# Optimization experiments

Measured on AMD Instinct MI355X. Metric: run time of the kernel, lower is better.

The kernel has to match this reference:

```python
import jax, jax.numpy as jnp
import numpy as np

CL = 256   # context_length (global in original code)
IL = 64    # inst_length (global in original code)
PC, CH1, CH2, CH3 = 64, 128, 256, 256
CK1, CK2, CK3 = 3, 3, 3
CS1, CS2, CS3 = 1, 2, 2
CP1, CP2, CP3 = 1, 1, 1
BCH1, BCH2, BCH3 = 64, 128, 256
F1, OUT = 1024, 2
B = 2048
C3_OUT = 64 * CH3            # 16384, per __init__ formula with CL-1=255
F1_IN = C3_OUT + BCH3        # 16640


def _conv1d(x, W, b, stride, pad):
    # x: [B, Cin, L], W: [Cout, Cin, K]
    y = jax.lax.conv_general_dilated(x, W, window_strides=(stride,),
                                     padding=[(pad, pad)],
                                     dimension_numbers=("NCH", "OIH", "NCH"))
    return y + b[None, :, None]


def setup_inputs() -> dict:
    key = jax.random.key(0)
    ks = jax.random.split(key, 20)
    s = lambda *sh: 1.0 / np.sqrt(np.prod(sh[1:]))
    def w(k, *sh):
        return jax.random.normal(k, sh, dtype=jnp.float32) * s(*sh)
    return {
        "x": jax.random.normal(ks[0], (B, CL * IL), dtype=jnp.float32),
        "Wp": w(ks[1], PC, IL, 2), "bp": jnp.zeros((PC,), jnp.float32),
        "W1": w(ks[2], CH1, PC, CK1), "b1": jnp.zeros((CH1,), jnp.float32),
        "W2": w(ks[3], CH2, CH1, CK2), "b2": jnp.zeros((CH2,), jnp.float32),
        "W3": w(ks[4], CH3, CH2, CK3), "b3": jnp.zeros((CH3,), jnp.float32),
        "Wb1": w(ks[5], BCH1, IL), "bb1": jnp.zeros((BCH1,), jnp.float32),
        "Wb2": w(ks[6], BCH2, BCH1), "bb2": jnp.zeros((BCH2,), jnp.float32),
        "Wb3": w(ks[7], BCH3, BCH2), "bb3": jnp.zeros((BCH3,), jnp.float32),
        "Wfc1": w(ks[8], F1, F1_IN), "bfc1": jnp.zeros((F1,), jnp.float32),
        "Wfc2": w(ks[9], OUT, F1), "bfc2": jnp.zeros((OUT,), jnp.float32),
    }


def reference(x, Wp, bp, W1, b1, W2, b2, W3, b3,
              Wb1, bb1, Wb2, bb2, Wb3, bb3, Wfc1, bfc1, Wfc2, bfc2):
    xr = x.reshape(-1, CL, IL).transpose(0, 2, 1)   # [B, IL, CL]
    x0 = xr[:, :, 0]                                 # [B, IL]
    # Fused replacement for the convp loop: kernel-2 conv over (x0, x_i)
    # y[:, :, i-1] = Wp[:,:,0] @ x0 + Wp[:,:,1] @ x_i + bp
    y = (jnp.einsum("bi,pi->bp", x0, Wp[:, :, 0])[:, :, None]
         + jnp.einsum("bic,pi->bpc", xr[:, :, 1:], Wp[:, :, 1])
         + bp[None, :, None])                        # [B, PC, CL-1]
    # bypass path on the first instruction (kernel-size-1 convs == matmuls)
    f = jax.nn.relu(x0 @ Wb1.T + bb1)
    f = jax.nn.relu(f @ Wb2.T + bb2)
    f = jax.nn.relu(f @ Wb3.T + bb3)                 # [B, BCH3]
    h = jax.nn.relu(y)
    h = jax.nn.relu(_conv1d(h, W1, b1, CS1, CP1))
    h = jax.nn.relu(_conv1d(h, W2, b2, CS2, CP2))
    h = jax.nn.relu(_conv1d(h, W3, b3, CS3, CP3))    # [B, CH3, 64]
    h = h.reshape(h.shape[0], C3_OUT)
    z = jnp.concatenate([h, f], axis=1)              # [B, F1_IN]
    z = jax.nn.relu(z @ Wfc1.T + bfc1)
    return z @ Wfc2.T + bfc2                         # [B, OUT]
```

## Files before the change

kernel.cpp:

```cpp
#include <hip/hip_runtime.h>
#include <cstdint>
#include <cstddef>

typedef __attribute__((ext_vector_type(8))) short bf16x8;
typedef __attribute__((ext_vector_type(8))) unsigned short ushort8;
typedef __attribute__((ext_vector_type(4))) float f32x4;

__device__ __forceinline__ unsigned short f2bf(float f){
  unsigned int u = __float_as_uint(f);
  unsigned int lsb = (u >> 16) & 1u;
  u += 0x7fffu + lsb;
  return (unsigned short)(u >> 16);
}

__device__ __forceinline__ void gload16(const void* g, void* l){
  __builtin_amdgcn_global_load_lds(
      (const __attribute__((address_space(1))) unsigned int*)g,
      (__attribute__((address_space(3))) unsigned int*)l, 16, 0, 0);
}

__global__ __launch_bounds__(256) void pack_w_bf16_kernel(const float* __restrict__ W,
    unsigned short* __restrict__ Wb, int COUT, int CIN){
  int idx = blockIdx.x*256 + threadIdx.x;
  int tot = COUT*CIN*3;
  if (idx >= tot) return;
  int o = idx/(CIN*3); int r = idx - o*(CIN*3); int kk = r/CIN; int ci = r - kk*CIN;
  Wb[idx] = f2bf(W[(o*CIN + ci)*3 + kk]);
}

__global__ __launch_bounds__(256) void pack_wp_kernel(const float* __restrict__ Wp,
                                                      unsigned short* __restrict__ Bw){
  int idx = blockIdx.x*256 + threadIdx.x;
  if (idx >= 64*128) return;
  int p = idx >> 7, k = idx & 127;
  float v = (k < 64) ? Wp[p*128 + k*2] : Wp[p*128 + (k-64)*2 + 1];
  Bw[idx] = f2bf(v);
}

__global__ __launch_bounds__(256) void f2bf_kernel(const float* __restrict__ src,
                                                   unsigned short* __restrict__ dst, int n){
  int i = blockIdx.x*256 + threadIdx.x;
  if (i < n) dst[i] = f2bf(src[i]);
}

__global__ __launch_bounds__(256) void zero_guards_kernel(unsigned short* __restrict__ buf,
                                                          int LINP, int CIN, int nb){
  int idx = blockIdx.x*256 + threadIdx.x;
  int per = 2*CIN/8;
  if (idx >= nb*per) return;
  int b = idx / per, r = idx - b*per;
  int g = r / (CIN/8), c8 = r - g*(CIN/8);
  ushort8 z = {0,0,0,0,0,0,0,0};
  *(ushort8*)(buf + ((size_t)b*LINP + (size_t)g*(LINP-1))*CIN + c8*8) = z;
}

__global__ __launch_bounds__(256) void branch_kernel(const float* __restrict__ x,
    const float* __restrict__ Wb1, const float* __restrict__ bb1,
    const float* __restrict__ Wb2, const float* __restrict__ bb2,
    const float* __restrict__ Wb3, const float* __restrict__ bb3,
    unsigned short* __restrict__ Hcat){
  __shared__ float s0[64], s1[64], s2[128];
  const int b = blockIdx.x, tid = threadIdx.x;
  const float* xb = x + (size_t)b*16384;
  if (tid < 64) s0[tid] = xb[tid];
  __syncthreads();
  if (tid < 64){
    float a = bb1[tid];
    for (int k=0;k<64;k++) a = fmaf(Wb1[tid*64+k], s0[k], a);
    s1[tid] = fmaxf(a, 0.f);
  }
  __syncthreads();
  if (tid < 128){
    float a = bb2[tid];
    for (int k=0;k<64;k++) a = fmaf(Wb2[tid*64+k], s1[k], a);
    s2[tid] = fmaxf(a, 0.f);
  }
  __syncthreads();
  float a = bb3[tid];
  for (int k=0;k<128;k++) a = fmaf(Wb3[tid*128+k], s2[k], a);
  Hcat[(size_t)b*16640 + 16384 + tid] = f2bf(fmaxf(a, 0.f));
}

__global__ __launch_bounds__(256) void h0_gemm_kernel(const float* __restrict__ x,
    const unsigned short* __restrict__ Bw, const float* __restrict__ bp,
    unsigned short* __restrict__ h0o){
  __shared__ __align__(16) char sAraw[128*256];
  __shared__ __align__(16) char sBraw[64*256];
  const int tid = threadIdx.x;
  const int m0 = blockIdx.x*128;
  #pragma unroll
  for (int i=0;i<16;i++){
    int j = tid + 256*i;
    int row = j >> 5, q = j & 31;
    int m = m0 + row;
    int b = m / 255, c = m - b*255;
    const float* xb = x + (size_t)b*16384;
    int k = q*4;
    const float* src = (k < 64) ? (xb + k) : (xb + (c+1)*64 + (k-64));
    float4 v = *(const float4*)src;
    ushort4 u; u.x=f2bf(v.x); u.y=f2bf(v.y); u.z=f2bf(v.z); u.w=f2bf(v.w);
    *(ushort4*)(sAraw + row*256 + ((k*2) ^ ((row&7)<<4))) = u;
  }
  #pragma unroll
  for (int i=0;i<4;i++){
    int j = tid + 256*i;
    int row = j >> 4, q = j & 15;
    int k = q*8;
    ushort8 u = *(const ushort8*)(Bw + row*128 + k);
    *(ushort8*)(sBraw + row*256 + ((k*2) ^ ((row&7)<<4))) = u;
  }
  __syncthreads();
  const int lane = tid & 63, wid = tid >> 6;
  const int lr = lane & 15, lg = lane >> 4;
  f32x4 acc[2][4];
  #pragma unroll
  for (int a=0;a<2;a++)
    #pragma unroll
    for (int j=0;j<4;j++) acc[a][j] = (f32x4){0,0,0,0};
  #pragma unroll
  for (int ks=0; ks<4; ks++){
    int k = ks*32 + lg*8;
    bf16x8 af[2], bfr[4];
    #pragma unroll
    for (int f=0; f<2; f++){
      int row = wid*32 + f*16 + lr;
      af[f] = *(const bf16x8*)(sAraw + row*256 + ((k*2) ^ ((row&7)<<4)));
    }
    #pragma unroll
    for (int f=0; f<4; f++){
      int row = f*16 + lr;
      bfr[f] = *(const bf16x8*)(sBraw + row*256 + ((k*2) ^ ((row&7)<<4)));
    }
    #pragma unroll
    for (int fi=0; fi<2; fi++)
      #pragma unroll
      for (int fj=0; fj<4; fj++)
        acc[fi][fj] = __builtin_amdgcn_mfma_f32_16x16x32_bf16(af[fi], bfr[fj], acc[fi][fj], 0,0,0);
  }
  #pragma unroll
  for (int fi=0; fi<2; fi++)
    #pragma unroll
    for (int fj=0; fj<4; fj++)
      #pragma unroll
      for (int j=0;j<4;j++){
        int m = m0 + wid*32 + fi*16 + lg*4 + j;
        int n = fj*16 + lr;
        int b = m / 255, t = m - b*255;
        h0o[((size_t)b*257 + t + 1)*64 + n] = f2bf(fmaxf(acc[fi][fj][j] + bp[n], 0.f));
      }
}

template<int CIN,int COUT,int S,int LOUT,int PADIN,int PADOUT,int BM,bool TO_HCAT>
__global__ __launch_bounds__(256) void conv_win_kernel(
    const unsigned short* __restrict__ in, const unsigned short* __restrict__ Wb,
    const float* __restrict__ bias, unsigned short* __restrict__ out){
  constexpr int K3  = 3*CIN, NCH = K3/64;
  constexpr int MPB = (LOUT + BM - 1)/BM;
  constexpr int NT  = COUT/128;
  constexpr int MF  = BM/32;
  constexpr int WR  = (BM-1)*S + 3;
  constexpr int CP8 = CIN/8;
  constexpr int CB  = CIN*2;
  constexpr int NSLOT = WR*CP8;
  __shared__ __align__(16) char SA[WR*CB];
  __shared__ __align__(16) char SB[2*16384];
  const int tid = threadIdx.x, lane = tid & 63, wid = tid >> 6;
  int lgid;
  { int bid = blockIdx.x, nwg = gridDim.x;
    lgid = ((nwg & 7)==0) ? ((bid & 7)*(nwg>>3) + (bid>>3)) : bid; }
  const int nt = lgid % NT;
  const int tile = lgid / NT;
  const int b = tile / MPB, mt = tile % MPB;
  const int t0 = mt*BM, n0 = nt*128;
  const unsigned short* Abase = in + ((size_t)b*PADIN + (size_t)t0*S)*CIN;
  const int rowlim = PADIN - t0*S;

  for (int i=0; i*256 < NSLOT; ++i){
    int slot = i*256 + tid;
    if (slot < NSLOT){
      int row = slot/CP8, p = slot - row*CP8;
      if (row < rowlim)
        gload16(Abase + (size_t)row*CIN + ((p ^ ((row>>(S-1))&7))<<3), SA + slot*16);
      else
        *(ushort8*)(SA + slot*16) = (ushort8){0,0,0,0,0,0,0,0};
    }
  }
  const int srow = lane >> 3;
  const int bsoff = (((lane&7) ^ srow) << 3);
  auto stageB = [&](int c, int bufi){
    #pragma unroll
    for (int s=0;s<4;s++){
      int row = wid*32 + s*8 + srow;
      gload16(Wb + (size_t)(n0+row)*K3 + c*64 + bsoff, SB + bufi*16384 + wid*4096 + s*1024);
    }
  };
  stageB(0, 0);
  __syncthreads();

  const int wm = wid >> 1, wn = wid & 1;
  const int lr = lane & 15, lg = lane >> 4;
  f32x4 acc[MF][4];
  #pragma unroll
  for (int i=0;i<MF;i++)
    #pragma unroll
    for (int j=0;j<4;j++) acc[i][j] = (f32x4){0,0,0,0};

  int buf = 0;
  #pragma unroll
  for (int c=0;c<NCH;c++){
    if (c+1 < NCH) stageB(c+1, buf^1);
    const int kk = c/(CIN/64), cc = c - kk*(CIN/64);
    #pragma unroll
    for (int ks=0; ks<2; ks++){
      bf16x8 af[MF], bfr[4];
      #pragma unroll
      for (int f=0;f<MF;f++){
        int row = (wm*(MF*16) + f*16 + lr)*S + kk;
        int ci = cc*8 + ks*4 + lg;
        af[f] = *(const bf16x8*)(SA + (size_t)row*CB + ((ci ^ ((row>>(S-1))&7))<<4));
      }
      #pragma unroll
      for (int f=0;f<4;f++){
        int rb = wn*64 + f*16 + lr;
        bfr[f] = *(const bf16x8*)(SB + buf*16384 + rb*128 + (((ks*4+lg) ^ (rb&7))<<4));
      }
      #pragma unroll
      for (int fi=0;fi<MF;fi++)
        #pragma unroll
        for (int fj=0;fj<4;fj++)
          acc[fi][fj] = __builtin_amdgcn_mfma_f32_16x16x32_bf16(af[fi], bfr[fj], acc[fi][fj], 0,0,0);
    }
    __syncthreads();
    buf ^= 1;
  }

  #pragma unroll
  for (int fi=0;fi<MF;fi++)
    #pragma unroll
    for (int fj=0;fj<4;fj++)
      #pragma unroll
      for (int j=0;j<4;j++){
        int t = t0 + wm*(MF*16) + fi*16 + lg*4 + j;
        int n = n0 + wn*64 + fj*16 + lr;
        if (MPB*BM == LOUT || t < LOUT){
          float v = fmaxf(acc[fi][fj][j] + bias[n], 0.f);
          if (TO_HCAT) out[(size_t)b*16640 + (size_t)n*64 + t] = f2bf(v);
          else         out[((size_t)b*PADOUT + t + 1)*COUT + n] = f2bf(v);
        }
      }
}

__global__ __launch_bounds__(256) void fc1_gemm_kernel(
    const unsigned short* __restrict__ A, const unsigned short* __restrict__ Bw,
    float* __restrict__ zp, int zoffm, int MT, int KZ){
  __shared__ __align__(16) char sA[2*128*128];
  __shared__ __align__(16) char sB[2*128*128];
  const int tid = threadIdx.x;
  const int nwg = gridDim.x;
  const int lgid = (blockIdx.x % 8)*(nwg/8) + blockIdx.x/8;
  const int kz  = lgid / (8*MT);
  const int rem = lgid % (8*MT);
  const int nt  = rem / MT;
  const int mt  = rem % MT;
  const int n0 = nt*128, m0 = mt*128;
  const int lane = tid & 63, wid = tid >> 6;
  const int wm = wid >> 1, wn = wid & 1;
  const int lr = lane & 15, lg = lane >> 4;
  const int srow = lane >> 3;
  const int soff = (((lane&7) ^ srow) << 3);
  f32x4 acc[4][4];
  #pragma unroll
  for (int i=0;i<4;i++)
    #pragma unroll
    for (int j=0;j<4;j++) acc[i][j] = (f32x4){0,0,0,0};
  const int it0 = (kz*260)/KZ, it1 = ((kz+1)*260)/KZ;

  auto stage = [&](int it, int bufi){
    const size_t k0 = (size_t)it*64;
    #pragma unroll
    for (int s=0;s<4;s++){
      int row = wid*32 + s*8 + srow;
      gload16(A  + (size_t)(m0+row)*16640 + k0 + soff, sA + bufi*16384 + wid*4096 + s*1024);
      gload16(Bw + (size_t)(n0+row)*16640 + k0 + soff, sB + bufi*16384 + wid*4096 + s*1024);
    }
  };
  stage(it0, 0);
  __syncthreads();
  int buf = 0;
  for (int it=it0; it<it1; ++it){
    if (it+1 < it1) stage(it+1, buf^1);
    #pragma unroll
    for (int ks=0; ks<2; ks++){
      const int k = ks*32 + lg*8;
      bf16x8 af[4], bfr[4];
      #pragma unroll
      for (int f=0;f<4;f++){
        int rowa = wm*64 + f*16 + lr;
        af[f]  = *(const bf16x8*)(sA + buf*16384 + rowa*128 + ((k*2) ^ ((rowa&7)<<4)));
        int rowb = wn*64 + f*16 + lr;
        bfr[f] = *(const bf16x8*)(sB + buf*16384 + rowb*128 + ((k*2) ^ ((rowb&7)<<4)));
      }
      #pragma unroll
      for (int fi=0;fi<4;fi++)
        #pragma unroll
        for (int fj=0;fj<4;fj++)
          acc[fi][fj] = __builtin_amdgcn_mfma_f32_16x16x32_bf16(af[fi], bfr[fj], acc[fi][fj], 0,0,0);
    }
    __syncthreads();
    buf ^= 1;
  }
  float* zo = zp + (size_t)kz*zoffm;
  #pragma unroll
  for (int fi=0;fi<4;fi++)
    #pragma unroll
    for (int fj=0;fj<4;fj++)
      #pragma unroll
      for (int j=0;j<4;j++){
        int m = m0 + wm*64 + fi*16 + lg*4 + j;
        int n = n0 + wn*64 + fj*16 + lr;
        zo[(size_t)m*1024 + n] = acc[fi][fj][j];
      }
}

__global__ __launch_bounds__(256) void fc2_kernel(const float* __restrict__ zp, int zoffm, int KZ,
    const float* __restrict__ bfc1, const float* __restrict__ Wfc2,
    const float* __restrict__ bfc2, float* __restrict__ out){
  __shared__ float red[4][2];
  const int b = blockIdx.x, tid = threadIdx.x;
  float a0 = 0.f, a1 = 0.f;
  for (int n = tid; n < 1024; n += 256){
    float s = bfc1[n];
    const float* zb = zp + (size_t)b*1024 + n;
    for (int kz = 0; kz < KZ; kz++) s += zb[(size_t)kz*zoffm];
    s = fmaxf(s, 0.f);
    a0 = fmaf(s, Wfc2[n], a0);
    a1 = fmaf(s, Wfc2[1024+n], a1);
  }
  #pragma unroll
  for (int m=32; m>=1; m>>=1){ a0 += __shfl_xor(a0, m, 64); a1 += __shfl_xor(a1, m, 64); }
  const int w = tid >> 6;
  if ((tid & 63) == 0){ red[w][0] = a0; red[w][1] = a1; }
  __syncthreads();
  if (tid == 0){
    out[(size_t)b*2]   = red[0][0]+red[1][0]+red[2][0]+red[3][0] + bfc2[0];
    out[(size_t)b*2+1] = red[0][1]+red[1][1]+red[2][1]+red[3][1] + bfc2[1];
  }
}

extern "C" void kernel_launch(void* const* d_in, const int* in_sizes, int n_in,
                              void* d_out, int out_size, void* d_ws, size_t ws_size,
                              hipStream_t stream){
  const float* x    = (const float*)d_in[0];
  const float* Wp   = (const float*)d_in[1];
  const float* bp   = (const float*)d_in[2];
  const float* W1   = (const float*)d_in[3];
  const float* b1   = (const float*)d_in[4];
  const float* W2   = (const float*)d_in[5];
  const float* b2   = (const float*)d_in[6];
  const float* W3   = (const float*)d_in[7];
  const float* b3   = (const float*)d_in[8];
  const float* Wb1  = (const float*)d_in[9];
  const float* bb1  = (const float*)d_in[10];
  const float* Wb2  = (const float*)d_in[11];
  const float* bb2  = (const float*)d_in[12];
  const float* Wb3  = (const float*)d_in[13];
  const float* bb3  = (const float*)d_in[14];
  const float* Wfc1 = (const float*)d_in[15];
  const float* bfc1 = (const float*)d_in[16];
  const float* Wfc2 = (const float*)d_in[17];
  const float* bfc2 = (const float*)d_in[18];
  float* out = (float*)d_out;

  size_t off = 0;
  char* basep = (char*)d_ws;
  auto carve = [&](size_t bytes)->char*{
    char* q = basep + off; off += (bytes + 255) & ~(size_t)255; return q;
  };
  unsigned short* W1b   = (unsigned short*)carve((size_t)128*3*64*2);
  unsigned short* W2b   = (unsigned short*)carve((size_t)256*3*128*2);
  unsigned short* W3b   = (unsigned short*)carve((size_t)256*3*256*2);
  unsigned short* Bwp   = (unsigned short*)carve((size_t)64*128*2);
  unsigned short* Wfc1b = (unsigned short*)carve((size_t)1024*16640*2);
  size_t fixed = off;

  int Bc = 128, KZ = 64;
  {
    const int bcs[5] = {2048, 1024, 512, 256, 128};
    const int kzs[5] = {4, 8, 16, 32, 64};
    for (int i = 0; i < 5; i++){
      size_t b = bcs[i];
      size_t need = fixed + b*((size_t)66560+65792+33280) + (size_t)kzs[i]*b*4096 + 16*256;
      if (need <= ws_size){ Bc = bcs[i]; KZ = kzs[i]; break; }
    }
  }
  const int NC = 2048/Bc;
  const int MT = Bc/128;
  unsigned short* buf1 = (unsigned short*)carve((size_t)Bc*66560);
  unsigned short* buf2 = (unsigned short*)carve((size_t)Bc*65792);
  unsigned short* Hcat = (unsigned short*)carve((size_t)Bc*33280);
  float*          zp   = (float*)carve((size_t)KZ*Bc*4096);
  const int zoffm = Bc*1024;

  hipLaunchKernelGGL(pack_w_bf16_kernel, dim3((128*64*3+255)/256), dim3(256), 0, stream, W1, W1b, 128, 64);
  hipLaunchKernelGGL(pack_w_bf16_kernel, dim3((256*128*3+255)/256), dim3(256), 0, stream, W2, W2b, 256, 128);
  hipLaunchKernelGGL(pack_w_bf16_kernel, dim3((256*256*3+255)/256), dim3(256), 0, stream, W3, W3b, 256, 256);
  hipLaunchKernelGGL(pack_wp_kernel, dim3(32), dim3(256), 0, stream, Wp, Bwp);
  hipLaunchKernelGGL(f2bf_kernel, dim3((17039360+255)/256), dim3(256), 0, stream, Wfc1, Wfc1b, 17039360);

  for (int c = 0; c < NC; ++c){
    const float* xc = x + (size_t)c*Bc*16384;
    hipLaunchKernelGGL(zero_guards_kernel, dim3((Bc*2*64/8+255)/256), dim3(256), 0, stream,
                       buf1, 257, 64, Bc);
    hipLaunchKernelGGL(zero_guards_kernel, dim3((Bc*2*128/8+255)/256), dim3(256), 0, stream,
                       buf2, 257, 128, Bc);
    hipLaunchKernelGGL(branch_kernel, dim3(Bc), dim3(256), 0, stream,
                       xc, Wb1, bb1, Wb2, bb2, Wb3, bb3, Hcat);
    hipLaunchKernelGGL(h0_gemm_kernel, dim3(Bc*255/128), dim3(256), 0, stream, xc, Bwp, bp, buf1);
    hipLaunchKernelGGL((conv_win_kernel<64,128,1,255,257,257,128,false>),
                       dim3(Bc*2), dim3(256), 0, stream, buf1, W1b, b1, buf2);
    hipLaunchKernelGGL(zero_guards_kernel, dim3((Bc*2*256/8+255)/256), dim3(256), 0, stream,
                       buf1, 130, 256, Bc);
    hipLaunchKernelGGL((conv_win_kernel<128,256,2,128,257,130,64,false>),
                       dim3(Bc*4), dim3(256), 0, stream, buf2, W2b, b2, buf1);
    hipLaunchKernelGGL((conv_win_kernel<256,256,2,64,130,0,32,true>),
                       dim3(Bc*4), dim3(256), 0, stream, buf1, W3b, b3, Hcat);
    hipLaunchKernelGGL(fc1_gemm_kernel, dim3(8*MT*KZ), dim3(256), 0, stream,
                       Hcat, Wfc1b, zp, zoffm, MT, KZ);
    hipLaunchKernelGGL(fc2_kernel, dim3(Bc), dim3(256), 0, stream,
                       zp, zoffm, KZ, bfc1, Wfc2, bfc2, out + (size_t)c*Bc*2);
  }
}
```

Measured before the change: 579.4 us.

## Rewrite conv layers as per-sample 512-thread kernels with register-resident weights

Replaces the windowed conv kernels, which split each sample into time tiles and staged weight chunks through double-buffered LDS, with one 512-thread block per sample. Each wave owns a slice of output channels and keeps its weights in registers, loading them in one or two halves. The whole padded input slab for a sample sits in LDS. This drops the per-chunk LDS weight staging and barriers and reads each input slab once, at the cost of heavy register pressure, fewer and larger blocks, and weights re-read from global or L2 by every block.

After: 568.3 us. No clear change (-1.9%).

```diff
diff --git a/kernel.cpp b/kernel.cpp
--- a/kernel.cpp
+++ b/kernel.cpp
@@ -150,100 +150,88 @@
       }
 }
 
-template<int CIN,int COUT,int S,int LOUT,int PADIN,int PADOUT,int BM,bool TO_HCAT>
-__global__ __launch_bounds__(256) void conv_win_kernel(
+template<int CIN,int COUT,int S,int LOUT,int PADIN,int PADOUT,int MF,int NF,int SLABROWS,bool TO_HCAT>
+__global__ __launch_bounds__(512, 2) void conv_bregw_kernel(
     const unsigned short* __restrict__ in, const unsigned short* __restrict__ Wb,
     const float* __restrict__ bias, unsigned short* __restrict__ out){
-  constexpr int K3  = 3*CIN, NCH = K3/64;
-  constexpr int MPB = (LOUT + BM - 1)/BM;
-  constexpr int NT  = COUT/128;
-  constexpr int MF  = BM/32;
-  constexpr int WR  = (BM-1)*S + 3;
-  constexpr int CP8 = CIN/8;
-  constexpr int CB  = CIN*2;
-  constexpr int NSLOT = WR*CP8;
-  __shared__ __align__(16) char SA[WR*CB];
-  __shared__ __align__(16) char SB[2*16384];
-  const int tid = threadIdx.x, lane = tid & 63, wid = tid >> 6;
-  int lgid;
-  { int bid = blockIdx.x, nwg = gridDim.x;
-    lgid = ((nwg & 7)==0) ? ((bid & 7)*(nwg>>3) + (bid>>3)) : bid; }
-  const int nt = lgid % NT;
-  const int tile = lgid / NT;
-  const int b = tile / MPB, mt = tile % MPB;
-  const int t0 = mt*BM, n0 = nt*128;
-  const unsigned short* Abase = in + ((size_t)b*PADIN + (size_t)t0*S)*CIN;
-  const int rowlim = PADIN - t0*S;
-
-  for (int i=0; i*256 < NSLOT; ++i){
-    int slot = i*256 + tid;
+  constexpr int K    = 3*CIN;
+  constexpr int NKS  = K/32;
+  constexpr int KSPLIT = (K > 384) ? 2 : 1;
+  constexpr int NKS_H  = NKS / KSPLIT;
+  constexpr int CP8  = CIN/8;
+  constexpr int CB   = CIN*2;
+  constexpr int NSLOT = SLABROWS*CP8;
+  __shared__ __align__(16) char SA[SLABROWS*CB];
+  const int tid = threadIdx.x, lane = tid & 63, wv = tid >> 6;
+  const int lr = lane & 15, lg = lane >> 4;
+  const int b = blockIdx.x;
+  const unsigned short* Abase = in + (size_t)b*PADIN*CIN;
+  const unsigned short* Wn = Wb + (size_t)(wv*(NF*16))*K;
+
+  #pragma unroll
+  for (int i=0; i*512 < NSLOT; ++i){
+    int slot = i*512 + tid;
     if (slot < NSLOT){
       int row = slot/CP8, p = slot - row*CP8;
-      if (row < rowlim)
-        gload16(Abase + (size_t)row*CIN + ((p ^ ((row>>(S-1))&7))<<3), SA + slot*16);
+      if (row < PADIN)
+        gload16(Abase + (size_t)row*CIN + (((p & 7) ^ ((row>>(S-1))&7))<<3) + (p & ~7)*8, SA + slot*16);
       else
         *(ushort8*)(SA + slot*16) = (ushort8){0,0,0,0,0,0,0,0};
     }
   }
-  const int srow = lane >> 3;
-  const int bsoff = (((lane&7) ^ srow) << 3);
-  auto stageB = [&](int c, int bufi){
-    #pragma unroll
-    for (int s=0;s<4;s++){
-      int row = wid*32 + s*8 + srow;
-      gload16(Wb + (size_t)(n0+row)*K3 + c*64 + bsoff, SB + bufi*16384 + wid*4096 + s*1024);
-    }
-  };
-  stageB(0, 0);
-  __syncthreads();
-
-  const int wm = wid >> 1, wn = wid & 1;
-  const int lr = lane & 15, lg = lane >> 4;
-  f32x4 acc[MF][4];
+
+  bf16x8 breg[NKS_H*NF];
+  #pragma unroll
+  for (int ks=0; ks<NKS_H; ks++)
+    #pragma unroll
+    for (int nf=0; nf<NF; nf++)
+      breg[ks*NF+nf] = *(const bf16x8*)(Wn + (size_t)(nf*16+lr)*K + ks*32 + lg*8);
+
+  __syncthreads();
+
+  f32x4 acc[MF][NF];
   #pragma unroll
   for (int i=0;i<MF;i++)
     #pragma unroll
-    for (int j=0;j<4;j++) acc[i][j] = (f32x4){0,0,0,0};
-
-  int buf = 0;
-  #pragma unroll
-  for (int c=0;c<NCH;c++){
-    if (c+1 < NCH) stageB(c+1, buf^1);
-    const int kk = c/(CIN/64), cc = c - kk*(CIN/64);
-    #pragma unroll
-    for (int ks=0; ks<2; ks++){
-      bf16x8 af[MF], bfr[4];
-      #pragma unroll
-      for (int f=0;f<MF;f++){
-        int row = (wm*(MF*16) + f*16 + lr)*S + kk;
-        int ci = cc*8 + ks*4 + lg;
-        af[f] = *(const bf16x8*)(SA + (size_t)row*CB + ((ci ^ ((row>>(S-1))&7))<<4));
+    for (int j=0;j<NF;j++) acc[i][j] = (f32x4){0,0,0,0};
+
+  #pragma unroll
+  for (int half=0; half<KSPLIT; half++){
+    if (half > 0){
+      #pragma unroll
+      for (int ks=0; ks<NKS_H; ks++)
+        #pragma unroll
+        for (int nf=0; nf<NF; nf++)
+          breg[ks*NF+nf] = *(const bf16x8*)(Wn + (size_t)(nf*16+lr)*K + half*(K/KSPLIT) + ks*32 + lg*8);
+    }
+    #pragma unroll
+    for (int ks=0; ks<NKS_H; ks++){
+      const int kglob = half*NKS_H + ks;
+      const int kk  = (kglob*32)/CIN;
+      const int ch0 = ((kglob*32)%CIN)/8;
+      #pragma unroll
+      for (int mf=0; mf<MF; mf++){
+        int row = (mf*16+lr)*S + kk;
+        int chunk = ch0 + lg;
+        bf16x8 af = *(const bf16x8*)(SA + (size_t)row*CB +
+                        ((((chunk & 7) ^ ((row>>(S-1))&7)) | (chunk & ~7)) << 4));
+        #pragma unroll
+        for (int nf=0; nf<NF; nf++)
+          acc[mf][nf] = __builtin_amdgcn_mfma_f32_16x16x32_bf16(af, breg[ks*NF+nf], acc[mf][nf], 0,0,0);
       }
-      #pragma unroll
-      for (int f=0;f<4;f++){
-        int rb = wn*64 + f*16 + lr;
-        bfr[f] = *(const bf16x8*)(SB + buf*16384 + rb*128 + (((ks*4+lg) ^ (rb&7))<<4));
-      }
-      #pragma unroll
-      for (int fi=0;fi<MF;fi++)
-        #pragma unroll
-        for (int fj=0;fj<4;fj++)
-          acc[fi][fj] = __builtin_amdgcn_mfma_f32_16x16x32_bf16(af[fi], bfr[fj], acc[fi][fj], 0,0,0);
-    }
-    __syncthreads();
-    buf ^= 1;
-  }
-
-  #pragma unroll
-  for (int fi=0;fi<MF;fi++)
-    #pragma unroll
-    for (int fj=0;fj<4;fj++)
+    }
+  }
+
+  #pragma unroll
+  for (int mf=0; mf<MF; mf++)
+    #pragma unroll
+    for (int nf=0; nf<NF; nf++)
       #pragma unroll
       for (int j=0;j<4;j++){
-        int t = t0 + wm*(MF*16) + fi*16 + lg*4 + j;
-        int n = n0 + wn*64 + fj*16 + lr;
-        if (MPB*BM == LOUT || t < LOUT){
-          float v = fmaxf(acc[fi][fj][j] + bias[n], 0.f);
+        int t = mf*16 + lg*4 + j;
+        int n = wv*(NF*16) + nf*16 + lr;
+        if (MF*16 == LOUT || t < LOUT){
+          float v = fmaxf(acc[mf][nf][j] + bias[n], 0.f);
           if (TO_HCAT) out[(size_t)b*16640 + (size_t)n*64 + t] = f2bf(v);
           else         out[((size_t)b*PADOUT + t + 1)*COUT + n] = f2bf(v);
         }
@@ -416,14 +404,14 @@
     hipLaunchKernelGGL(branch_kernel, dim3(Bc), dim3(256), 0, stream,
                        xc, Wb1, bb1, Wb2, bb2, Wb3, bb3, Hcat);
     hipLaunchKernelGGL(h0_gemm_kernel, dim3(Bc*255/128), dim3(256), 0, stream, xc, Bwp, bp, buf1);
-    hipLaunchKernelGGL((conv_win_kernel<64,128,1,255,257,257,128,false>),
-                       dim3(Bc*2), dim3(256), 0, stream, buf1, W1b, b1, buf2);
+    hipLaunchKernelGGL((conv_bregw_kernel<64,128,1,255,257,257,16,1,259,false>),
+                       dim3(Bc), dim3(512), 0, stream, buf1, W1b, b1, buf2);
     hipLaunchKernelGGL(zero_guards_kernel, dim3((Bc*2*256/8+255)/256), dim3(256), 0, stream,
                        buf1, 130, 256, Bc);
-    hipLaunchKernelGGL((conv_win_kernel<128,256,2,128,257,130,64,false>),
-                       dim3(Bc*4), dim3(256), 0, stream, buf2, W2b, b2, buf1);
-    hipLaunchKernelGGL((conv_win_kernel<256,256,2,64,130,0,32,true>),
-                       dim3(Bc*4), dim3(256), 0, stream, buf1, W3b, b3, Hcat);
+    hipLaunchKernelGGL((conv_bregw_kernel<128,256,2,128,257,130,8,2,257,false>),
+                       dim3(Bc), dim3(512), 0, stream, buf2, W2b, b2, buf1);
+    hipLaunchKernelGGL((conv_bregw_kernel<256,256,2,64,130,0,4,2,130,true>),
+                       dim3(Bc), dim3(512), 0, stream, buf1, W3b, b3, Hcat);
     hipLaunchKernelGGL(fc1_gemm_kernel, dim3(8*MT*KZ), dim3(256), 0, stream,
                        Hcat, Wfc1b, zp, zoffm, MT, KZ);
     hipLaunchKernelGGL(fc2_kernel, dim3(Bc), dim3(256), 0, stream,
```
